# Performance work log

Hardware: AMD Instinct MI355X
Metric: run time of the kernel (lower is better)

The kernel has to match this reference:

```python
import jax, jax.numpy as jnp
import numpy as np

D, NH, NKV, HD, DFF, W, PLD = 2048, 8, 2, 256, 8192, 512, 256
EPS = 1e-6

def rmsnorm(x, w):
    # Gemma-style RMSNorm with (1 + weight) scaling
    return x * jax.lax.rsqrt(jnp.mean(x * x, axis=-1, keepdims=True) + EPS) * (1.0 + w)

def rmsnorm_nw(x):
    # v_norm: weightless RMSNorm
    return x * jax.lax.rsqrt(jnp.mean(x * x, axis=-1, keepdims=True) + EPS)

def rotate_half(x):
    x1, x2 = jnp.split(x, 2, axis=-1)
    return jnp.concatenate([-x2, x1], axis=-1)

def setup_inputs() -> dict:
    key = jax.random.key(0)
    ks = jax.random.split(key, 24)
    w = lambda k, shp, s=0.02: (jax.random.normal(k, shp, dtype=jnp.float32) * s)
    inp = {
        "hidden_states": jax.random.normal(ks[0], (1, 1, D), dtype=jnp.float32),
        "cos": jax.random.uniform(ks[1], (1, 1, HD), dtype=jnp.float32),
        "sin": jax.random.uniform(ks[2], (1, 1, HD), dtype=jnp.float32),
        "mask": jnp.zeros((1, 1, 1, W), dtype=jnp.float32),
        "kv_cache": jnp.zeros((2, NKV, W, HD), dtype=jnp.float32),
        "per_layer": jax.random.normal(ks[3], (1, 1, PLD), dtype=jnp.float32),
        "ln_in_w": w(ks[4], (D,)),
        "Wq": w(ks[5], (NH * HD, D)),
        "q_norm_w": w(ks[6], (HD,)),
        "Wk": w(ks[7], (NKV * HD, D)),
        "Wv": w(ks[8], (NKV * HD, D)),
        "k_norm_w": w(ks[9], (HD,)),
        "Wo": w(ks[10], (D, NH * HD)),
        "post_attn_ln_w": w(ks[11], (D,)),
        "pre_ffn_ln_w": w(ks[12], (D,)),
        "Wgate": w(ks[13], (DFF, D)),
        "Wup": w(ks[14], (DFF, D)),
        "Wdown": w(ks[15], (D, DFF)),
        "post_ffn_ln_w": w(ks[16], (D,)),
        "Wpl_gate": w(ks[17], (PLD, D)),
        "Wpl_proj": w(ks[18], (D, PLD)),
        "post_pl_ln_w": w(ks[19], (D,)),
        "layer_scalar": jnp.ones((1,), dtype=jnp.float32),
        "ring_pos": 37,
    }
    return inp

def reference(hidden_states, cos, sin, mask, kv_cache, per_layer,
              ln_in_w, Wq, q_norm_w, Wk, Wv, k_norm_w, Wo,
              post_attn_ln_w, pre_ffn_ln_w, Wgate, Wup, Wdown, post_ffn_ln_w,
              Wpl_gate, Wpl_proj, post_pl_ln_w, layer_scalar, ring_pos):
    n_rep = NH // NKV
    x = hidden_states[0, 0]                      # (D,)
    residual = x
    h = rmsnorm(x, ln_in_w)                      # input_layernorm
    c, s = cos[0, 0], sin[0, 0]                  # (HD,)
    # q/k/v projections (seq=1 decode -> GEMV)
    q = (h @ Wq.T).reshape(NH, HD)
    q = rmsnorm(q, q_norm_w)
    q = q * c + rotate_half(q) * s               # RoPE
    k = (h @ Wk.T).reshape(NKV, HD)
    k = rmsnorm(k, k_norm_w)
    k = k * c + rotate_half(k) * s
    v = rmsnorm_nw((h @ Wv.T).reshape(NKV, HD))
    # slice-write into the ring-buffer KV cache
    kv = kv_cache.at[0, :, ring_pos, :].set(k).at[1, :, ring_pos, :].set(v)
    K, V = kv[0], kv[1]                          # (NKV, W, HD)
    # GQA: repeat kv heads n_rep times
    Kx = jnp.repeat(K, n_rep, axis=0)            # (NH, W, HD)
    Vx = jnp.repeat(V, n_rep, axis=0)
    scores = jnp.einsum('hd,hwd->hw', q, Kx) + mask[0, 0, 0]   # no 1/sqrt(hd), as in source
    attn = jax.nn.softmax(scores, axis=-1)
    o = jnp.einsum('hw,hwd->hd', attn, Vx).reshape(NH * HD)
    attn_out = rmsnorm(o @ Wo.T, post_attn_ln_w)
    x = residual + attn_out
    # gated-GELU MLP
    residual = x
    hn = rmsnorm(x, pre_ffn_ln_w)
    gate = jax.nn.gelu(hn @ Wgate.T, approximate=True)
    mlp = ((gate * (hn @ Wup.T)) @ Wdown.T)
    x = residual + rmsnorm(mlp, post_ffn_ln_w)
    # per-layer input gate/projection
    residual = x
    g = jax.nn.gelu(x @ Wpl_gate.T, approximate=True) * per_layer[0, 0]
    g = rmsnorm(g @ Wpl_proj.T, post_pl_ln_w)
    x = (residual + g) * layer_scalar[0]
    return x.reshape(1, 1, D)

if __name__ == '__main__':
    out = reference(**setup_inputs())
    print(out.shape, out.dtype)
```

## Files before the change

### kernel.cpp

```cpp
#include <hip/hip_runtime.h>
#include <math.h>

#define D 2048
#define NH 8
#define NKV 2
#define HD 256
#define DFF 8192
#define W 512
#define PLD 256
#define EPS 1e-6f

__device__ __forceinline__ float warp_sum(float v) {
    #pragma unroll
    for (int off = 32; off > 0; off >>= 1) v += __shfl_down(v, off, 64);
    return v;
}
__device__ __forceinline__ float warp_max(float v) {
    #pragma unroll
    for (int off = 32; off > 0; off >>= 1) v = fmaxf(v, __shfl_down(v, off, 64));
    return v;
}

__device__ __forceinline__ float block_sum256(float v, float* s4) {
    int lane = threadIdx.x & 63, wid = threadIdx.x >> 6;
    v = warp_sum(v);
    if (lane == 0) s4[wid] = v;
    __syncthreads();
    float r = s4[0] + s4[1] + s4[2] + s4[3];
    __syncthreads();
    return r;
}
__device__ __forceinline__ float block_max256(float v, float* s4) {
    int lane = threadIdx.x & 63, wid = threadIdx.x >> 6;
    v = warp_max(v);
    if (lane == 0) s4[wid] = v;
    __syncthreads();
    float r = fmaxf(fmaxf(s4[0], s4[1]), fmaxf(s4[2], s4[3]));
    __syncthreads();
    return r;
}

__device__ __forceinline__ float gelu_tanh(float x) {
    const float c = 0.7978845608028654f;
    float t = tanhf(c * (x + 0.044715f * x * x * x));
    return 0.5f * x * (1.0f + t);
}

__global__ void rms_in_kernel(const float* __restrict__ x, const float* __restrict__ w,
                              float* __restrict__ out) {
    __shared__ float s4[4];
    int t = threadIdx.x;
    float v[8], ss = 0.f;
    #pragma unroll
    for (int i = 0; i < 8; i++) { v[i] = x[t + i * 256]; ss += v[i] * v[i]; }
    float tot = block_sum256(ss, s4);
    float rs = rsqrtf(tot / (float)D + EPS);
    #pragma unroll
    for (int i = 0; i < 8; i++) out[t + i * 256] = v[i] * rs * (1.f + w[t + i * 256]);
}

__global__ void gemv_qkv(const float* __restrict__ Wq, const float* __restrict__ Wk,
                         const float* __restrict__ Wv, const float* __restrict__ h,
                         float* __restrict__ qraw, float* __restrict__ kraw,
                         float* __restrict__ vraw) {
    int lane = threadIdx.x & 63, wid = threadIdx.x >> 6;
    int row = blockIdx.x * 4 + wid;
    const float* wr;
    float* out;
    if (row < 2048)      { wr = Wq + (size_t)row * D;          out = qraw + row; }
    else if (row < 2560) { wr = Wk + (size_t)(row - 2048) * D; out = kraw + (row - 2048); }
    else                 { wr = Wv + (size_t)(row - 2560) * D; out = vraw + (row - 2560); }
    float acc = 0.f;
    #pragma unroll 4
    for (int it = 0; it < D / 256; it++) {
        int c = it * 256 + lane * 4;
        float4 wv = *reinterpret_cast<const float4*>(wr + c);
        float4 hv = *reinterpret_cast<const float4*>(h + c);
        acc = fmaf(wv.x, hv.x, fmaf(wv.y, hv.y, fmaf(wv.z, hv.z, fmaf(wv.w, hv.w, acc))));
    }
    acc = warp_sum(acc);
    if (lane == 0) *out = acc;
}

__global__ void head_norm_rope(const float* __restrict__ qraw, const float* __restrict__ kraw,
                               const float* __restrict__ vraw, const float* __restrict__ qw,
                               const float* __restrict__ kw, const float* __restrict__ cosv,
                               const float* __restrict__ sinv, float* __restrict__ qf,
                               float* __restrict__ kf, float* __restrict__ vf) {
    __shared__ float s4[4];
    __shared__ float sn[HD];
    int b = blockIdx.x, t = threadIdx.x;
    const float* in; float* out; const float* w; bool rope;
    if (b < 8)       { in = qraw + b * HD;        out = qf + b * HD;        w = qw;      rope = true;  }
    else if (b < 10) { in = kraw + (b - 8) * HD;  out = kf + (b - 8) * HD;  w = kw;      rope = true;  }
    else             { in = vraw + (b - 10) * HD; out = vf + (b - 10) * HD; w = nullptr; rope = false; }
    float x = in[t];
    float tot = block_sum256(x * x, s4);
    float rs = rsqrtf(tot / (float)HD + EPS);
    float nv = x * rs * (w ? (1.f + w[t]) : 1.f);
    sn[t] = nv;
    __syncthreads();
    float o = nv;
    if (rope) {
        float rh = (t < HD / 2) ? -sn[t + HD / 2] : sn[t - HD / 2];
        o = nv * cosv[t] + rh * sinv[t];
    }
    out[t] = o;
}

__global__ void attn_scores(const float* __restrict__ kvc, const float* __restrict__ kf,
                            const float* __restrict__ mask, const float* __restrict__ qf,
                            const int* __restrict__ ring_p, float* __restrict__ scores) {
    int head = blockIdx.x >> 3, wc = blockIdx.x & 7;
    int kvh = head >> 2;
    int lane = threadIdx.x & 63, wid = threadIdx.x >> 6;
    int ring = *ring_p;
    float4 qv = *reinterpret_cast<const float4*>(qf + head * HD + lane * 4);
    const float* Kbase = kvc + (size_t)kvh * W * HD;
    #pragma unroll 4
    for (int i = 0; i < 16; i++) {
        int w = wc * 64 + wid * 16 + i;
        const float* krow = (w == ring) ? (kf + kvh * HD) : (Kbase + (size_t)w * HD);
        float4 kv4 = *reinterpret_cast<const float4*>(krow + lane * 4);
        float acc = qv.x * kv4.x + qv.y * kv4.y + qv.z * kv4.z + qv.w * kv4.w;
        acc = warp_sum(acc);
        if (lane == 0) scores[head * W + w] = acc + mask[w];
    }
}

__global__ void attn_softmax(float* __restrict__ scores, float* __restrict__ attn_o) {
    __shared__ float s4[4];
    int head = blockIdx.x, t = threadIdx.x;
    float s0 = scores[head * W + t], s1 = scores[head * W + 256 + t];
    float m = block_max256(fmaxf(s0, s1), s4);
    float e0 = expf(s0 - m), e1 = expf(s1 - m);
    float sum = block_sum256(e0 + e1, s4);
    float inv = 1.f / sum;
    scores[head * W + t] = e0 * inv;
    scores[head * W + 256 + t] = e1 * inv;
    attn_o[head * HD + t] = 0.f;
}

__global__ void attn_o_partial(const float* __restrict__ kvc, const float* __restrict__ vf,
                               const float* __restrict__ p, const int* __restrict__ ring_p,
                               float* __restrict__ attn_o) {
    int head = blockIdx.x >> 3, wc = blockIdx.x & 7;
    int kvh = head >> 2;
    int d = threadIdx.x;
    int ring = *ring_p;
    const float* Vbase = kvc + (size_t)(NKV + kvh) * W * HD;
    float acc = 0.f;
    #pragma unroll 4
    for (int i = 0; i < 64; i++) {
        int w = wc * 64 + i;
        float pw = p[head * W + w];
        const float* vrow = (w == ring) ? (vf + kvh * HD) : (Vbase + (size_t)w * HD);
        acc = fmaf(pw, vrow[d], acc);
    }
    atomicAdd(&attn_o[head * HD + d], acc);
}

template <int NC>
__global__ void gemv(const float* __restrict__ Wm, const float* __restrict__ x,
                     float* __restrict__ y) {
    int lane = threadIdx.x & 63, wid = threadIdx.x >> 6;
    int row = blockIdx.x * 4 + wid;
    const float* wr = Wm + (size_t)row * NC;
    float acc = 0.f;
    #pragma unroll 4
    for (int it = 0; it < NC / 256; it++) {
        int c = it * 256 + lane * 4;
        float4 wv = *reinterpret_cast<const float4*>(wr + c);
        float4 xv = *reinterpret_cast<const float4*>(x + c);
        acc = fmaf(wv.x, xv.x, fmaf(wv.y, xv.y, fmaf(wv.z, xv.z, fmaf(wv.w, xv.w, acc))));
    }
    acc = warp_sum(acc);
    if (lane == 0) y[row] = acc;
}

__global__ void gemv_gateup(const float* __restrict__ Wg, const float* __restrict__ Wu,
                            const float* __restrict__ hn, float* __restrict__ act) {
    int lane = threadIdx.x & 63, wid = threadIdx.x >> 6;
    int row = blockIdx.x * 4 + wid;
    const float* wg = Wg + (size_t)row * D;
    const float* wu = Wu + (size_t)row * D;
    float accg = 0.f, accu = 0.f;
    #pragma unroll 4
    for (int it = 0; it < D / 256; it++) {
        int c = it * 256 + lane * 4;
        float4 hv = *reinterpret_cast<const float4*>(hn + c);
        float4 gv = *reinterpret_cast<const float4*>(wg + c);
        float4 uv = *reinterpret_cast<const float4*>(wu + c);
        accg = fmaf(gv.x, hv.x, fmaf(gv.y, hv.y, fmaf(gv.z, hv.z, fmaf(gv.w, hv.w, accg))));
        accu = fmaf(uv.x, hv.x, fmaf(uv.y, hv.y, fmaf(uv.z, hv.z, fmaf(uv.w, hv.w, accu))));
    }
    accg = warp_sum(accg);
    accu = warp_sum(accu);
    if (lane == 0) act[row] = gelu_tanh(accg) * accu;
}

__global__ void gemv_plgate(const float* __restrict__ Wm, const float* __restrict__ x,
                            const float* __restrict__ per_layer, float* __restrict__ g) {
    int lane = threadIdx.x & 63, wid = threadIdx.x >> 6;
    int row = blockIdx.x * 4 + wid;
    const float* wr = Wm + (size_t)row * D;
    float acc = 0.f;
    #pragma unroll 4
    for (int it = 0; it < D / 256; it++) {
        int c = it * 256 + lane * 4;
        float4 wv = *reinterpret_cast<const float4*>(wr + c);
        float4 xv = *reinterpret_cast<const float4*>(x + c);
        acc = fmaf(wv.x, xv.x, fmaf(wv.y, xv.y, fmaf(wv.z, xv.z, fmaf(wv.w, xv.w, acc))));
    }
    acc = warp_sum(acc);
    if (lane == 0) g[row] = gelu_tanh(acc) * per_layer[row];
}

__global__ void post_attn_fused(const float* __restrict__ res, const float* __restrict__ y,
                                const float* __restrict__ w1, const float* __restrict__ w2,
                                float* __restrict__ x1, float* __restrict__ hn) {
    __shared__ float s4[4];
    int t = threadIdx.x;
    float yv[8], ss = 0.f;
    #pragma unroll
    for (int i = 0; i < 8; i++) { yv[i] = y[t + i * 256]; ss += yv[i] * yv[i]; }
    float tot = block_sum256(ss, s4);
    float rs = rsqrtf(tot / (float)D + EPS);
    float xv[8]; ss = 0.f;
    #pragma unroll
    for (int i = 0; i < 8; i++) {
        int idx = t + i * 256;
        float v = res[idx] + yv[i] * rs * (1.f + w1[idx]);
        xv[i] = v; x1[idx] = v; ss += v * v;
    }
    tot = block_sum256(ss, s4);
    rs = rsqrtf(tot / (float)D + EPS);
    #pragma unroll
    for (int i = 0; i < 8; i++) {
        int idx = t + i * 256;
        hn[idx] = xv[i] * rs * (1.f + w2[idx]);
    }
}

__global__ void residual_rms(const float* __restrict__ res, const float* __restrict__ y,
                             const float* __restrict__ w, float* __restrict__ out) {
    __shared__ float s4[4];
    int t = threadIdx.x;
    float yv[8], ss = 0.f;
    #pragma unroll
    for (int i = 0; i < 8; i++) { yv[i] = y[t + i * 256]; ss += yv[i] * yv[i]; }
    float tot = block_sum256(ss, s4);
    float rs = rsqrtf(tot / (float)D + EPS);
    #pragma unroll
    for (int i = 0; i < 8; i++) {
        int idx = t + i * 256;
        out[idx] = res[idx] + yv[i] * rs * (1.f + w[idx]);
    }
}

__global__ void final_kernel(const float* __restrict__ x2, const float* __restrict__ g2,
                             const float* __restrict__ w, const float* __restrict__ scal,
                             float* __restrict__ out) {
    __shared__ float s4[4];
    int t = threadIdx.x;
    float gv[8], ss = 0.f;
    #pragma unroll
    for (int i = 0; i < 8; i++) { gv[i] = g2[t + i * 256]; ss += gv[i] * gv[i]; }
    float tot = block_sum256(ss, s4);
    float rs = rsqrtf(tot / (float)D + EPS);
    float sc = scal[0];
    #pragma unroll
    for (int i = 0; i < 8; i++) {
        int idx = t + i * 256;
        out[idx] = (x2[idx] + gv[i] * rs * (1.f + w[idx])) * sc;
    }
}

extern "C" void kernel_launch(void* const* d_in, const int* in_sizes, int n_in,
                              void* d_out, int out_size, void* d_ws, size_t ws_size,
                              hipStream_t stream) {
    const float* x_in        = (const float*)d_in[0];
    const float* cosv        = (const float*)d_in[1];
    const float* sinv        = (const float*)d_in[2];
    const float* mask        = (const float*)d_in[3];
    const float* kvc         = (const float*)d_in[4];
    const float* per_layer   = (const float*)d_in[5];
    const float* ln_in_w     = (const float*)d_in[6];
    const float* Wq          = (const float*)d_in[7];
    const float* q_norm_w    = (const float*)d_in[8];
    const float* Wk          = (const float*)d_in[9];
    const float* Wv          = (const float*)d_in[10];
    const float* k_norm_w    = (const float*)d_in[11];
    const float* Wo          = (const float*)d_in[12];
    const float* post_attn_w = (const float*)d_in[13];
    const float* pre_ffn_w   = (const float*)d_in[14];
    const float* Wgate       = (const float*)d_in[15];
    const float* Wup         = (const float*)d_in[16];
    const float* Wdown       = (const float*)d_in[17];
    const float* post_ffn_w  = (const float*)d_in[18];
    const float* Wpl_gate    = (const float*)d_in[19];
    const float* Wpl_proj    = (const float*)d_in[20];
    const float* post_pl_w   = (const float*)d_in[21];
    const float* layer_scal  = (const float*)d_in[22];
    const int*   ring_pos    = (const int*)d_in[23];
    float* out = (float*)d_out;
    float* ws  = (float*)d_ws;

    float* h      = ws;
    float* qraw   = ws + 2048;
    float* kraw   = ws + 4096;
    float* vraw   = ws + 4608;
    float* qf     = ws + 5120;
    float* kf     = ws + 7168;
    float* vf     = ws + 7680;
    float* scores = ws + 8192;
    float* attn_o = ws + 12288;
    float* y_wo   = ws + 14336;
    float* x1     = ws + 16384;
    float* hn     = ws + 18432;
    float* act    = ws + 20480;
    float* y2     = ws + 28672;
    float* x2     = ws + 30720;
    float* g      = ws + 32768;
    float* g2     = ws + 33024;

    rms_in_kernel<<<1, 256, 0, stream>>>(x_in, ln_in_w, h);
    gemv_qkv<<<768, 256, 0, stream>>>(Wq, Wk, Wv, h, qraw, kraw, vraw);
    head_norm_rope<<<12, 256, 0, stream>>>(qraw, kraw, vraw, q_norm_w, k_norm_w,
                                           cosv, sinv, qf, kf, vf);
    attn_scores<<<64, 256, 0, stream>>>(kvc, kf, mask, qf, ring_pos, scores);
    attn_softmax<<<8, 256, 0, stream>>>(scores, attn_o);
    attn_o_partial<<<64, 256, 0, stream>>>(kvc, vf, scores, ring_pos, attn_o);
    gemv<2048><<<512, 256, 0, stream>>>(Wo, attn_o, y_wo);
    post_attn_fused<<<1, 256, 0, stream>>>(x_in, y_wo, post_attn_w, pre_ffn_w, x1, hn);
    gemv_gateup<<<2048, 256, 0, stream>>>(Wgate, Wup, hn, act);
    gemv<8192><<<512, 256, 0, stream>>>(Wdown, act, y2);
    residual_rms<<<1, 256, 0, stream>>>(x1, y2, post_ffn_w, x2);
    gemv_plgate<<<64, 256, 0, stream>>>(Wpl_gate, x2, per_layer, g);
    gemv<256><<<512, 256, 0, stream>>>(Wpl_proj, g, g2);
    final_kernel<<<1, 256, 0, stream>>>(x2, g2, post_pl_w, layer_scal, out);
}
```

Baseline: 82.23 us.

## Stage GEMV weight rows into LDS via direct global-to-LDS loads

```diff
diff --git a/kernel.cpp b/kernel.cpp
--- a/kernel.cpp
+++ b/kernel.cpp
@@ -46,6 +46,11 @@
     return 0.5f * x * (1.0f + t);
 }
 
+__device__ __forceinline__ void stage16(const float* g, float* l) {
+    __builtin_amdgcn_global_load_lds((const __attribute__((address_space(1))) void*)g,
+                                     (__attribute__((address_space(3))) void*)l, 16, 0, 0);
+}
+
 __global__ void rms_in_kernel(const float* __restrict__ x, const float* __restrict__ w,
                               float* __restrict__ out) {
     __shared__ float s4[4];
@@ -59,27 +64,184 @@
     for (int i = 0; i < 8; i++) out[t + i * 256] = v[i] * rs * (1.f + w[t + i * 256]);
 }
 
-__global__ void gemv_qkv(const float* __restrict__ Wq, const float* __restrict__ Wk,
-                         const float* __restrict__ Wv, const float* __restrict__ h,
-                         float* __restrict__ qraw, float* __restrict__ kraw,
-                         float* __restrict__ vraw) {
+__global__ void gemv_qkv_lds(const float* __restrict__ Wq, const float* __restrict__ Wk,
+                             const float* __restrict__ Wv, const float* __restrict__ h,
+                             float* __restrict__ qraw, float* __restrict__ kraw,
+                             float* __restrict__ vraw) {
+    __shared__ float smem[4 * 2048];
     int lane = threadIdx.x & 63, wid = threadIdx.x >> 6;
     int row = blockIdx.x * 4 + wid;
+    float* buf = smem + wid * 2048;
     const float* wr;
     float* out;
     if (row < 2048)      { wr = Wq + (size_t)row * D;          out = qraw + row; }
     else if (row < 2560) { wr = Wk + (size_t)(row - 2048) * D; out = kraw + (row - 2048); }
     else                 { wr = Wv + (size_t)(row - 2560) * D; out = vraw + (row - 2560); }
+    #pragma unroll
+    for (int c = 0; c < 8; c++) stage16(wr + c * 256 + lane * 4, buf + c * 256);
+    float4 xv[8];
+    #pragma unroll
+    for (int c = 0; c < 8; c++) xv[c] = *reinterpret_cast<const float4*>(h + c * 256 + lane * 4);
+    asm volatile("s_waitcnt vmcnt(0)" ::: "memory");
     float acc = 0.f;
-    #pragma unroll 4
-    for (int it = 0; it < D / 256; it++) {
-        int c = it * 256 + lane * 4;
-        float4 wv = *reinterpret_cast<const float4*>(wr + c);
-        float4 hv = *reinterpret_cast<const float4*>(h + c);
-        acc = fmaf(wv.x, hv.x, fmaf(wv.y, hv.y, fmaf(wv.z, hv.z, fmaf(wv.w, hv.w, acc))));
+    #pragma unroll
+    for (int c = 0; c < 8; c++) {
+        float4 wv = *reinterpret_cast<float4*>(buf + c * 256 + lane * 4);
+        acc = fmaf(wv.x, xv[c].x, fmaf(wv.y, xv[c].y, fmaf(wv.z, xv[c].z, fmaf(wv.w, xv[c].w, acc))));
     }
     acc = warp_sum(acc);
     if (lane == 0) *out = acc;
+}
+
+template <int MODE>
+__global__ void gemv2048_lds(const float* __restrict__ Wm, const float* __restrict__ x,
+                             const float* __restrict__ aux, float* __restrict__ y) {
+    __shared__ float smem[4 * 2048];
+    int lane = threadIdx.x & 63, wid = threadIdx.x >> 6;
+    int row = blockIdx.x * 4 + wid;
+    float* buf = smem + wid * 2048;
+    const float* wr = Wm + (size_t)row * D;
+    #pragma unroll
+    for (int c = 0; c < 8; c++) stage16(wr + c * 256 + lane * 4, buf + c * 256);
+    float4 xv[8];
+    #pragma unroll
+    for (int c = 0; c < 8; c++) xv[c] = *reinterpret_cast<const float4*>(x + c * 256 + lane * 4);
+    asm volatile("s_waitcnt vmcnt(0)" ::: "memory");
+    float acc = 0.f;
+    #pragma unroll
+    for (int c = 0; c < 8; c++) {
+        float4 wv = *reinterpret_cast<float4*>(buf + c * 256 + lane * 4);
+        acc = fmaf(wv.x, xv[c].x, fmaf(wv.y, xv[c].y, fmaf(wv.z, xv[c].z, fmaf(wv.w, xv[c].w, acc))));
+    }
+    acc = warp_sum(acc);
+    if (lane == 0) {
+        if (MODE == 0) y[row] = acc;
+        else           y[row] = gelu_tanh(acc) * aux[row];
+    }
+}
+
+__global__ void gateup_lds(const float* __restrict__ Wg, const float* __restrict__ Wu,
+                           const float* __restrict__ hn, float* __restrict__ act) {
+    __shared__ float smem[4 * 2048];
+    int lane = threadIdx.x & 63, wid = threadIdx.x >> 6;
+    int row = blockIdx.x * 4 + wid;
+    float* bufA = smem + wid * 2048;
+    float* bufB = bufA + 1024;
+    const float* wg = Wg + (size_t)row * D;
+    const float* wu = Wu + (size_t)row * D;
+    float4 xv[8];
+    #pragma unroll
+    for (int c = 0; c < 8; c++) xv[c] = *reinterpret_cast<const float4*>(hn + c * 256 + lane * 4);
+    #pragma unroll
+    for (int i = 0; i < 2; i++) stage16(wg + (0 + i) * 256 + lane * 4, bufA + i * 256);
+    #pragma unroll
+    for (int i = 0; i < 2; i++) stage16(wu + (0 + i) * 256 + lane * 4, bufA + 512 + i * 256);
+    #pragma unroll
+    for (int i = 0; i < 2; i++) stage16(wg + (2 + i) * 256 + lane * 4, bufB + i * 256);
+    #pragma unroll
+    for (int i = 0; i < 2; i++) stage16(wu + (2 + i) * 256 + lane * 4, bufB + 512 + i * 256);
+    float ag = 0.f, au = 0.f;
+    asm volatile("s_waitcnt vmcnt(4)" ::: "memory");
+    #pragma unroll
+    for (int i = 0; i < 2; i++) {
+        float4 gv = *reinterpret_cast<float4*>(bufA + i * 256 + lane * 4);
+        float4 uv = *reinterpret_cast<float4*>(bufA + 512 + i * 256 + lane * 4);
+        float4 x4 = xv[0 * 2 + i];
+        ag = fmaf(gv.x, x4.x, fmaf(gv.y, x4.y, fmaf(gv.z, x4.z, fmaf(gv.w, x4.w, ag))));
+        au = fmaf(uv.x, x4.x, fmaf(uv.y, x4.y, fmaf(uv.z, x4.z, fmaf(uv.w, x4.w, au))));
+    }
+    #pragma unroll
+    for (int i = 0; i < 2; i++) stage16(wg + (4 + i) * 256 + lane * 4, bufA + i * 256);
+    #pragma unroll
+    for (int i = 0; i < 2; i++) stage16(wu + (4 + i) * 256 + lane * 4, bufA + 512 + i * 256);
+    asm volatile("s_waitcnt vmcnt(4)" ::: "memory");
+    #pragma unroll
+    for (int i = 0; i < 2; i++) {
+        float4 gv = *reinterpret_cast<float4*>(bufB + i * 256 + lane * 4);
+        float4 uv = *reinterpret_cast<float4*>(bufB + 512 + i * 256 + lane * 4);
+        float4 x4 = xv[1 * 2 + i];
+        ag = fmaf(gv.x, x4.x, fmaf(gv.y, x4.y, fmaf(gv.z, x4.z, fmaf(gv.w, x4.w, ag))));
+        au = fmaf(uv.x, x4.x, fmaf(uv.y, x4.y, fmaf(uv.z, x4.z, fmaf(uv.w, x4.w, au))));
+    }
+    #pragma unroll
+    for (int i = 0; i < 2; i++) stage16(wg + (6 + i) * 256 + lane * 4, bufB + i * 256);
+    #pragma unroll
+    for (int i = 0; i < 2; i++) stage16(wu + (6 + i) * 256 + lane * 4, bufB + 512 + i * 256);
+    asm volatile("s_waitcnt vmcnt(4)" ::: "memory");
+    #pragma unroll
+    for (int i = 0; i < 2; i++) {
+        float4 gv = *reinterpret_cast<float4*>(bufA + i * 256 + lane * 4);
+        float4 uv = *reinterpret_cast<float4*>(bufA + 512 + i * 256 + lane * 4);
+        float4 x4 = xv[2 * 2 + i];
+        ag = fmaf(gv.x, x4.x, fmaf(gv.y, x4.y, fmaf(gv.z, x4.z, fmaf(gv.w, x4.w, ag))));
+        au = fmaf(uv.x, x4.x, fmaf(uv.y, x4.y, fmaf(uv.z, x4.z, fmaf(uv.w, x4.w, au))));
+    }
+    asm volatile("s_waitcnt vmcnt(0)" ::: "memory");
+    #pragma unroll
+    for (int i = 0; i < 2; i++) {
+        float4 gv = *reinterpret_cast<float4*>(bufB + i * 256 + lane * 4);
+        float4 uv = *reinterpret_cast<float4*>(bufB + 512 + i * 256 + lane * 4);
+        float4 x4 = xv[3 * 2 + i];
+        ag = fmaf(gv.x, x4.x, fmaf(gv.y, x4.y, fmaf(gv.z, x4.z, fmaf(gv.w, x4.w, ag))));
+        au = fmaf(uv.x, x4.x, fmaf(uv.y, x4.y, fmaf(uv.z, x4.z, fmaf(uv.w, x4.w, au))));
+    }
+    ag = warp_sum(ag);
+    au = warp_sum(au);
+    if (lane == 0) act[row] = gelu_tanh(ag) * au;
+}
+
+__global__ void down_lds(const float* __restrict__ Wd, const float* __restrict__ act,
+                         float* __restrict__ y) {
+    __shared__ float smem[4 * 4096];
+    int lane = threadIdx.x & 63, wid = threadIdx.x >> 6;
+    int row = blockIdx.x * 4 + wid;
+    float* bufA = smem + wid * 4096;
+    float* bufB = bufA + 2048;
+    const float* wr = Wd + (size_t)row * DFF;
+    float4 av[8];
+    float acc = 0.f;
+    #pragma unroll
+    for (int c = 0; c < 8; c++) stage16(wr + c * 256 + lane * 4, bufA + c * 256);
+    #pragma unroll
+    for (int c = 0; c < 8; c++) av[c] = *reinterpret_cast<const float4*>(act + c * 256 + lane * 4);
+    #pragma unroll
+    for (int c = 0; c < 8; c++) stage16(wr + 2048 + c * 256 + lane * 4, bufB + c * 256);
+    asm volatile("s_waitcnt vmcnt(8)" ::: "memory");
+    #pragma unroll
+    for (int c = 0; c < 8; c++) {
+        float4 wv = *reinterpret_cast<float4*>(bufA + c * 256 + lane * 4);
+        acc = fmaf(wv.x, av[c].x, fmaf(wv.y, av[c].y, fmaf(wv.z, av[c].z, fmaf(wv.w, av[c].w, acc))));
+    }
+    #pragma unroll
+    for (int c = 0; c < 8; c++) av[c] = *reinterpret_cast<const float4*>(act + 2048 + c * 256 + lane * 4);
+    #pragma unroll
+    for (int c = 0; c < 8; c++) stage16(wr + 4096 + c * 256 + lane * 4, bufA + c * 256);
+    asm volatile("s_waitcnt vmcnt(8)" ::: "memory");
+    #pragma unroll
+    for (int c = 0; c < 8; c++) {
+        float4 wv = *reinterpret_cast<float4*>(bufB + c * 256 + lane * 4);
+        acc = fmaf(wv.x, av[c].x, fmaf(wv.y, av[c].y, fmaf(wv.z, av[c].z, fmaf(wv.w, av[c].w, acc))));
+    }
+    #pragma unroll
+    for (int c = 0; c < 8; c++) av[c] = *reinterpret_cast<const float4*>(act + 4096 + c * 256 + lane * 4);
+    #pragma unroll
+    for (int c = 0; c < 8; c++) stage16(wr + 6144 + c * 256 + lane * 4, bufB + c * 256);
+    asm volatile("s_waitcnt vmcnt(8)" ::: "memory");
+    #pragma unroll
+    for (int c = 0; c < 8; c++) {
+        float4 wv = *reinterpret_cast<float4*>(bufA + c * 256 + lane * 4);
+        acc = fmaf(wv.x, av[c].x, fmaf(wv.y, av[c].y, fmaf(wv.z, av[c].z, fmaf(wv.w, av[c].w, acc))));
+    }
+    #pragma unroll
+    for (int c = 0; c < 8; c++) av[c] = *reinterpret_cast<const float4*>(act + 6144 + c * 256 + lane * 4);
+    asm volatile("s_waitcnt vmcnt(0)" ::: "memory");
+    #pragma unroll
+    for (int c = 0; c < 8; c++) {
+        float4 wv = *reinterpret_cast<float4*>(bufB + c * 256 + lane * 4);
+        acc = fmaf(wv.x, av[c].x, fmaf(wv.y, av[c].y, fmaf(wv.z, av[c].z, fmaf(wv.w, av[c].w, acc))));
+    }
+    acc = warp_sum(acc);
+    if (lane == 0) y[row] = acc;
 }
 
 __global__ void head_norm_rope(const float* __restrict__ qraw, const float* __restrict__ kraw,
@@ -167,7 +329,7 @@
     int row = blockIdx.x * 4 + wid;
     const float* wr = Wm + (size_t)row * NC;
     float acc = 0.f;
-    #pragma unroll 4
+    #pragma unroll
     for (int it = 0; it < NC / 256; it++) {
         int c = it * 256 + lane * 4;
         float4 wv = *reinterpret_cast<const float4*>(wr + c);
@@ -176,44 +338,6 @@
     }
     acc = warp_sum(acc);
     if (lane == 0) y[row] = acc;
-}
-
-__global__ void gemv_gateup(const float* __restrict__ Wg, const float* __restrict__ Wu,
-                            const float* __restrict__ hn, float* __restrict__ act) {
-    int lane = threadIdx.x & 63, wid = threadIdx.x >> 6;
-    int row = blockIdx.x * 4 + wid;
-    const float* wg = Wg + (size_t)row * D;
-    const float* wu = Wu + (size_t)row * D;
-    float accg = 0.f, accu = 0.f;
-    #pragma unroll 4
-    for (int it = 0; it < D / 256; it++) {
-        int c = it * 256 + lane * 4;
-        float4 hv = *reinterpret_cast<const float4*>(hn + c);
-        float4 gv = *reinterpret_cast<const float4*>(wg + c);
-        float4 uv = *reinterpret_cast<const float4*>(wu + c);
-        accg = fmaf(gv.x, hv.x, fmaf(gv.y, hv.y, fmaf(gv.z, hv.z, fmaf(gv.w, hv.w, accg))));
-        accu = fmaf(uv.x, hv.x, fmaf(uv.y, hv.y, fmaf(uv.z, hv.z, fmaf(uv.w, hv.w, accu))));
-    }
-    accg = warp_sum(accg);
-    accu = warp_sum(accu);
-    if (lane == 0) act[row] = gelu_tanh(accg) * accu;
-}
-
-__global__ void gemv_plgate(const float* __restrict__ Wm, const float* __restrict__ x,
-                            const float* __restrict__ per_layer, float* __restrict__ g) {
-    int lane = threadIdx.x & 63, wid = threadIdx.x >> 6;
-    int row = blockIdx.x * 4 + wid;
-    const float* wr = Wm + (size_t)row * D;
-    float acc = 0.f;
-    #pragma unroll 4
-    for (int it = 0; it < D / 256; it++) {
-        int c = it * 256 + lane * 4;
-        float4 wv = *reinterpret_cast<const float4*>(wr + c);
-        float4 xv = *reinterpret_cast<const float4*>(x + c);
-        acc = fmaf(wv.x, xv.x, fmaf(wv.y, xv.y, fmaf(wv.z, xv.z, fmaf(wv.w, xv.w, acc))));
-    }
-    acc = warp_sum(acc);
-    if (lane == 0) g[row] = gelu_tanh(acc) * per_layer[row];
 }
 
 __global__ void post_attn_fused(const float* __restrict__ res, const float* __restrict__ y,
@@ -325,18 +449,18 @@
     float* g2     = ws + 33024;
 
     rms_in_kernel<<<1, 256, 0, stream>>>(x_in, ln_in_w, h);
-    gemv_qkv<<<768, 256, 0, stream>>>(Wq, Wk, Wv, h, qraw, kraw, vraw);
+    gemv_qkv_lds<<<768, 256, 0, stream>>>(Wq, Wk, Wv, h, qraw, kraw, vraw);
     head_norm_rope<<<12, 256, 0, stream>>>(qraw, kraw, vraw, q_norm_w, k_norm_w,
                                            cosv, sinv, qf, kf, vf);
     attn_scores<<<64, 256, 0, stream>>>(kvc, kf, mask, qf, ring_pos, scores);
     attn_softmax<<<8, 256, 0, stream>>>(scores, attn_o);
     attn_o_partial<<<64, 256, 0, stream>>>(kvc, vf, scores, ring_pos, attn_o);
-    gemv<2048><<<512, 256, 0, stream>>>(Wo, attn_o, y_wo);
+    gemv2048_lds<0><<<512, 256, 0, stream>>>(Wo, attn_o, nullptr, y_wo);
     post_attn_fused<<<1, 256, 0, stream>>>(x_in, y_wo, post_attn_w, pre_ffn_w, x1, hn);
-    gemv_gateup<<<2048, 256, 0, stream>>>(Wgate, Wup, hn, act);
-    gemv<8192><<<512, 256, 0, stream>>>(Wdown, act, y2);
+    gateup_lds<<<2048, 256, 0, stream>>>(Wgate, Wup, hn, act);
+    down_lds<<<512, 256, 0, stream>>>(Wdown, act, y2);
     residual_rms<<<1, 256, 0, stream>>>(x1, y2, post_ffn_w, x2);
-    gemv_plgate<<<64, 256, 0, stream>>>(Wpl_gate, x2, per_layer, g);
+    gemv2048_lds<1><<<64, 256, 0, stream>>>(Wpl_gate, x2, per_layer, g);
     gemv<256><<<512, 256, 0, stream>>>(Wpl_proj, g, g2);
     final_kernel<<<1, 256, 0, stream>>>(x2, g2, post_pl_w, layer_scal, out);
 }
```

Result: no change. 83.13 us (+1.1%).
